# Optimization experiments

Measured on AMD Instinct MI355X. Metric: run time of the kernel, lower is better.

## Reference

```python
import jax, jax.numpy as jnp
import numpy as np

B, L, E = 8, 2048, 4096
TOKEN_DIM, EDGE_DIM, HIDDEN = 768, 256, 128


def setup_inputs() -> dict:
    key = jax.random.key(0)
    k1, k2, k3, k4, k5 = jax.random.split(key, 5)
    token_embedding = jax.random.normal(k1, (B, L, TOKEN_DIM), dtype=jnp.float32)
    edge_embedding = jax.random.normal(k2, (B, E, EDGE_DIM), dtype=jnp.float32)
    # fc: Linear(token_dim+edge_dim -> hidden, bias=False); stored as [in, out]
    W_fc = jax.random.normal(k3, (TOKEN_DIM + EDGE_DIM, HIDDEN), dtype=jnp.float32) * 0.02
    # attn_fc: Linear(2*hidden -> 1); weight flattened to [2*hidden], plus scalar bias
    a_attn = jax.random.normal(k4, (2 * HIDDEN,), dtype=jnp.float32) * 0.02
    b_attn = jax.random.normal(k5, (1,), dtype=jnp.float32) * 0.02
    return {"token_embedding": token_embedding, "edge_embedding": edge_embedding,
            "W_fc": W_fc, "a_attn": a_attn, "b_attn": b_attn}


def reference(token_embedding, edge_embedding, W_fc, a_attn, b_attn):
    # avg edge embedding, broadcast over sequence
    avg_edge = edge_embedding.mean(axis=1, keepdims=True)          # [B, 1, De]
    avg_edge = jnp.broadcast_to(avg_edge, (token_embedding.shape[0],
                                           token_embedding.shape[1],
                                           avg_edge.shape[-1]))     # [B, L, De]
    combined = jnp.concatenate([token_embedding, avg_edge], axis=-1)  # [B, L, Dt+De]
    h = jnp.einsum('bld,dh->blh', combined, W_fc)                   # [B, L, H]

    # Additive attention decomposition: a^T [h_j || h_i] = a1.h_j + a2.h_i
    # (original builds concat([h_repeat_row (=h_j), h_repeat_col (=h_i)]))
    H = h.shape[-1]
    a1, a2 = a_attn[:H], a_attn[H:]
    s_j = jnp.einsum('blh,h->bl', h, a1)                            # score contrib from h_j
    s_i = jnp.einsum('blh,h->bl', h, a2)                            # score contrib from h_i
    scores = s_i[:, :, None] + s_j[:, None, :] + b_attn[0]          # [B, L, L], scores[b,i,j]
    attn = jax.nn.softmax(scores, axis=-1)                          # softmax over j
    h_prime = jnp.einsum('bij,bjh->bih', attn, h)                   # [B, L, H]
    return h_prime
```

## Files before the change

kernel.cpp:

```cpp
#include <hip/hip_runtime.h>

constexpr int Bn  = 8;
constexpr int Ln  = 2048;
constexpr int En  = 4096;
constexpr int TDn = 768;
constexpr int EDn = 256;
constexpr int Hn  = 128;

constexpr int OFF_V1   = 0;
constexpr int OFF_TREC = 1024;
constexpr int TRECF    = 772;
constexpr int OFF_EREC = OFF_TREC + 512 * TRECF;

__global__ __launch_bounds__(256)
void K_0(const float* __restrict__ W, const float* __restrict__ a,
         float* __restrict__ ws)
{
    const int tid = threadIdx.x, wv = tid >> 6, lane = tid & 63;
    int d = blockIdx.x * 4 + wv;
    float acc = W[d * Hn + lane]      * a[lane]
              + W[d * Hn + 64 + lane] * a[64 + lane];
    #pragma unroll
    for (int off = 32; off > 0; off >>= 1)
        acc += __shfl_down(acc, off, 64);
    if (lane == 0) ws[OFF_V1 + d] = acc;
}

__global__ __launch_bounds__(256)
void K_1(const float* __restrict__ token, const float* __restrict__ edge,
         float* __restrict__ ws)
{
    const int tid = threadIdx.x, wv = tid >> 6, lane = tid & 63;
    const int bi = blockIdx.x;
    __shared__ __align__(16) float4 smf[4 * 192];
    __shared__ float sm_den[4];

    if (bi < 512) {
        const int b = bi >> 6, chunk = bi & 63;
        const size_t row0 = (size_t)b * Ln + chunk * 32 + wv * 8;

        const float4* v1_4 = (const float4*)(ws + OFF_V1);
        float4 u0 = v1_4[lane], u1 = v1_4[64 + lane], u2 = v1_4[128 + lane];

        float4 a0 = {0,0,0,0}, a1 = {0,0,0,0}, a2 = {0,0,0,0};
        float esum = 0.f;
        const float4* t4 = (const float4*)token + row0 * (TDn / 4);
        #pragma unroll
        for (int i = 0; i < 8; ++i) {
            float4 v0 = t4[i * 192 + lane];
            float4 v1 = t4[i * 192 + 64 + lane];
            float4 v2 = t4[i * 192 + 128 + lane];
            float d = v0.x*u0.x + v0.y*u0.y + v0.z*u0.z + v0.w*u0.w
                    + v1.x*u1.x + v1.y*u1.y + v1.z*u1.z + v1.w*u1.w
                    + v2.x*u2.x + v2.y*u2.y + v2.z*u2.z + v2.w*u2.w;
            #pragma unroll
            for (int off = 32; off > 0; off >>= 1)
                d += __shfl_xor(d, off, 64);
            float e = expf(d);
            esum += e;
            a0.x += e*v0.x; a0.y += e*v0.y; a0.z += e*v0.z; a0.w += e*v0.w;
            a1.x += e*v1.x; a1.y += e*v1.y; a1.z += e*v1.z; a1.w += e*v1.w;
            a2.x += e*v2.x; a2.y += e*v2.y; a2.z += e*v2.z; a2.w += e*v2.w;
        }
        smf[wv * 192 + lane]       = a0;
        smf[wv * 192 + 64 + lane]  = a1;
        smf[wv * 192 + 128 + lane] = a2;
        if (lane == 0) sm_den[wv] = esum;
        __syncthreads();

        float* rec = ws + OFF_TREC + (size_t)bi * TRECF;
        if (tid < 192) {
            float4 r  = smf[tid];
            float4 r1 = smf[192 + tid], r2 = smf[384 + tid], r3 = smf[576 + tid];
            r.x += r1.x + r2.x + r3.x;  r.y += r1.y + r2.y + r3.y;
            r.z += r1.z + r2.z + r3.z;  r.w += r1.w + r2.w + r3.w;
            ((float4*)(rec + 4))[tid] = r;
        }
        if (tid == 0)
            rec[0] = sm_den[0] + sm_den[1] + sm_den[2] + sm_den[3];
    } else {
        const int eb = bi - 512;
        const int b = eb >> 6, chunk = eb & 63;
        const size_t row0 = (size_t)b * En + chunk * 64 + wv * 16;
        const float4* e4 = (const float4*)edge + row0 * (EDn / 4) + lane;
        float4 acc = {0,0,0,0};
        #pragma unroll
        for (int i = 0; i < 16; ++i) {
            float4 v = e4[(size_t)i * (EDn / 4)];
            acc.x += v.x; acc.y += v.y; acc.z += v.z; acc.w += v.w;
        }
        smf[wv * 64 + lane] = acc;
        __syncthreads();
        if (tid < 64) {
            float4 r0 = smf[tid],       r1 = smf[64 + tid],
                   r2 = smf[128 + tid], r3 = smf[192 + tid];
            float4 s = {r0.x + r1.x + r2.x + r3.x, r0.y + r1.y + r2.y + r3.y,
                        r0.z + r1.z + r2.z + r3.z, r0.w + r1.w + r2.w + r3.w};
            ((float4*)(ws + OFF_EREC))[(size_t)eb * 64 + tid] = s;
        }
    }
}

__global__ __launch_bounds__(256)
void K_2(const float* __restrict__ W, const float* __restrict__ ws,
         float4* __restrict__ out)
{
    __shared__ __align__(16) float s_c[1024];
    __shared__ __align__(16) float4 smp[256];
    __shared__ __align__(16) float4 s_row[32];
    __shared__ float s_den;
    const int tid = threadIdx.x;
    const int b = blockIdx.x >> 5, slice = blockIdx.x & 31;

    float dpart = (tid < 64)
        ? ws[OFF_TREC + (size_t)(b * 64 + tid) * TRECF] : 0.f;

    float4 acc = {0,0,0,0};
    if (tid < 192) {
        const float4* rb = (const float4*)(ws + OFF_TREC)
                         + (size_t)(b * 64) * (TRECF / 4) + 1 + tid;
        #pragma unroll 8
        for (int k = 0; k < 64; ++k) {
            float4 v = rb[(size_t)k * (TRECF / 4)];
            acc.x += v.x; acc.y += v.y; acc.z += v.z; acc.w += v.w;
        }
    } else {
        const float4* rb = (const float4*)(ws + OFF_EREC)
                         + (size_t)(b * 64) * (EDn / 4) + (tid - 192);
        #pragma unroll 8
        for (int k = 0; k < 64; ++k) {
            float4 v = rb[(size_t)k * (EDn / 4)];
            acc.x += v.x; acc.y += v.y; acc.z += v.z; acc.w += v.w;
        }
    }
    if (tid < 64) {
        #pragma unroll
        for (int off = 32; off > 0; off >>= 1)
            dpart += __shfl_xor(dpart, off, 64);
        if (tid == 0) s_den = dpart;
    }
    __syncthreads();

    float scale = (tid < 192) ? (1.0f / s_den) : (1.0f / En);
    float4 c = {acc.x * scale, acc.y * scale, acc.z * scale, acc.w * scale};
    ((float4*)s_c)[tid] = c;
    __syncthreads();

    const int hq = tid & 31, dg = tid >> 5;
    const float4* W4 = (const float4*)W;
    const float* cp = s_c + dg * 128;
    float4 m = {0,0,0,0};
    #pragma unroll 8
    for (int i = 0; i < 128; ++i) {
        float cv = cp[i];
        float4 w = W4[(size_t)(dg * 128 + i) * (Hn / 4) + hq];
        m.x += cv * w.x; m.y += cv * w.y; m.z += cv * w.z; m.w += cv * w.w;
    }
    smp[tid] = m;
    __syncthreads();
    if (tid < 32) {
        float4 r = smp[tid];
        #pragma unroll
        for (int g = 1; g < 8; ++g) {
            float4 v = smp[g * 32 + tid];
            r.x += v.x; r.y += v.y; r.z += v.z; r.w += v.w;
        }
        s_row[tid] = r;
    }
    __syncthreads();

    float4* ob = out + ((size_t)b * Ln + slice * 64) * (Hn / 4);
    #pragma unroll
    for (int k = 0; k < 8; ++k) {
        int f = k * 256 + tid;
        ob[f] = s_row[f & 31];
    }
}

extern "C" void kernel_launch(void* const* d_in, const int* in_sizes, int n_in,
                              void* d_out, int out_size, void* d_ws, size_t ws_size,
                              hipStream_t stream) {
    const float* token = (const float*)d_in[0];
    const float* edge  = (const float*)d_in[1];
    const float* W     = (const float*)d_in[2];
    const float* a     = (const float*)d_in[3];
    float* ws   = (float*)d_ws;
    float4* out = (float4*)d_out;

    K_0<<<192,  256, 0, stream>>>(W, a, ws);
    K_1<<<1024, 256, 0, stream>>>(token, edge, ws);
    K_2<<<256,  256, 0, stream>>>(W, ws, out);
}
```

Before: 128.9 us.

## Fuse token and edge work into uniform blocks with batched loads

K_1 stops splitting blocks into token-only and edge-only branches. Each of the 1024 blocks now handles 16 token rows and 32 edge rows, issues all its token loads up front, and runs four independent dot-product and shuffle reductions together to expose more memory-level parallelism. Because the number of partial records per batch doubles, K_2 reduces 128 records per batch and runs with fewer blocks that each write more output rows. The aim is better load balance and latency hiding in the bandwidth-bound pass, at the cost of a longer reduction in K_2 and more register pressure.

```diff
diff --git a/kernel.cpp b/kernel.cpp
--- a/kernel.cpp
+++ b/kernel.cpp
@@ -10,7 +10,7 @@
 constexpr int OFF_V1   = 0;
 constexpr int OFF_TREC = 1024;
 constexpr int TRECF    = 772;
-constexpr int OFF_EREC = OFF_TREC + 512 * TRECF;
+constexpr int OFF_EREC = OFF_TREC + 1024 * TRECF;
 
 __global__ __launch_bounds__(256)
 void K_0(const float* __restrict__ W, const float* __restrict__ a,
@@ -26,78 +26,108 @@
     if (lane == 0) ws[OFF_V1 + d] = acc;
 }
 
-__global__ __launch_bounds__(256)
+__global__ __launch_bounds__(256, 4)
 void K_1(const float* __restrict__ token, const float* __restrict__ edge,
          float* __restrict__ ws)
 {
     const int tid = threadIdx.x, wv = tid >> 6, lane = tid & 63;
     const int bi = blockIdx.x;
+    const int b = bi >> 7, chunk = bi & 127;
     __shared__ __align__(16) float4 smf[4 * 192];
+    __shared__ __align__(16) float4 sme[4 * 64];
     __shared__ float sm_den[4];
 
-    if (bi < 512) {
-        const int b = bi >> 6, chunk = bi & 63;
-        const size_t row0 = (size_t)b * Ln + chunk * 32 + wv * 8;
-
-        const float4* v1_4 = (const float4*)(ws + OFF_V1);
-        float4 u0 = v1_4[lane], u1 = v1_4[64 + lane], u2 = v1_4[128 + lane];
-
-        float4 a0 = {0,0,0,0}, a1 = {0,0,0,0}, a2 = {0,0,0,0};
-        float esum = 0.f;
-        const float4* t4 = (const float4*)token + row0 * (TDn / 4);
-        #pragma unroll
-        for (int i = 0; i < 8; ++i) {
-            float4 v0 = t4[i * 192 + lane];
-            float4 v1 = t4[i * 192 + 64 + lane];
-            float4 v2 = t4[i * 192 + 128 + lane];
-            float d = v0.x*u0.x + v0.y*u0.y + v0.z*u0.z + v0.w*u0.w
-                    + v1.x*u1.x + v1.y*u1.y + v1.z*u1.z + v1.w*u1.w
-                    + v2.x*u2.x + v2.y*u2.y + v2.z*u2.z + v2.w*u2.w;
-            #pragma unroll
-            for (int off = 32; off > 0; off >>= 1)
-                d += __shfl_xor(d, off, 64);
-            float e = expf(d);
-            esum += e;
-            a0.x += e*v0.x; a0.y += e*v0.y; a0.z += e*v0.z; a0.w += e*v0.w;
-            a1.x += e*v1.x; a1.y += e*v1.y; a1.z += e*v1.z; a1.w += e*v1.w;
-            a2.x += e*v2.x; a2.y += e*v2.y; a2.z += e*v2.z; a2.w += e*v2.w;
-        }
-        smf[wv * 192 + lane]       = a0;
-        smf[wv * 192 + 64 + lane]  = a1;
-        smf[wv * 192 + 128 + lane] = a2;
-        if (lane == 0) sm_den[wv] = esum;
-        __syncthreads();
-
-        float* rec = ws + OFF_TREC + (size_t)bi * TRECF;
-        if (tid < 192) {
-            float4 r  = smf[tid];
-            float4 r1 = smf[192 + tid], r2 = smf[384 + tid], r3 = smf[576 + tid];
-            r.x += r1.x + r2.x + r3.x;  r.y += r1.y + r2.y + r3.y;
-            r.z += r1.z + r2.z + r3.z;  r.w += r1.w + r2.w + r3.w;
-            ((float4*)(rec + 4))[tid] = r;
-        }
-        if (tid == 0)
-            rec[0] = sm_den[0] + sm_den[1] + sm_den[2] + sm_den[3];
-    } else {
-        const int eb = bi - 512;
-        const int b = eb >> 6, chunk = eb & 63;
-        const size_t row0 = (size_t)b * En + chunk * 64 + wv * 16;
-        const float4* e4 = (const float4*)edge + row0 * (EDn / 4) + lane;
-        float4 acc = {0,0,0,0};
-        #pragma unroll
-        for (int i = 0; i < 16; ++i) {
-            float4 v = e4[(size_t)i * (EDn / 4)];
-            acc.x += v.x; acc.y += v.y; acc.z += v.z; acc.w += v.w;
-        }
-        smf[wv * 64 + lane] = acc;
-        __syncthreads();
-        if (tid < 64) {
-            float4 r0 = smf[tid],       r1 = smf[64 + tid],
-                   r2 = smf[128 + tid], r3 = smf[192 + tid];
-            float4 s = {r0.x + r1.x + r2.x + r3.x, r0.y + r1.y + r2.y + r3.y,
-                        r0.z + r1.z + r2.z + r3.z, r0.w + r1.w + r2.w + r3.w};
-            ((float4*)(ws + OFF_EREC))[(size_t)eb * 64 + tid] = s;
-        }
+    const float4* v1_4 = (const float4*)(ws + OFF_V1);
+    float4 u0 = v1_4[lane], u1 = v1_4[64 + lane], u2 = v1_4[128 + lane];
+
+    const size_t trow0 = (size_t)b * Ln + chunk * 16 + wv * 4;
+    const float4* t4 = (const float4*)token + trow0 * (TDn / 4);
+    float4 r0[4], r1[4], r2[4];
+    #pragma unroll
+    for (int i = 0; i < 4; ++i) {
+        r0[i] = t4[i * 192 + lane];
+        r1[i] = t4[i * 192 + 64 + lane];
+        r2[i] = t4[i * 192 + 128 + lane];
+    }
+
+    float d0, d1, d2, d3;
+    {
+        float4 *p;
+        p = &r0[0];
+        d0 = p->x*u0.x + p->y*u0.y + p->z*u0.z + p->w*u0.w;
+        p = &r1[0]; d0 += p->x*u1.x + p->y*u1.y + p->z*u1.z + p->w*u1.w;
+        p = &r2[0]; d0 += p->x*u2.x + p->y*u2.y + p->z*u2.z + p->w*u2.w;
+        p = &r0[1];
+        d1 = p->x*u0.x + p->y*u0.y + p->z*u0.z + p->w*u0.w;
+        p = &r1[1]; d1 += p->x*u1.x + p->y*u1.y + p->z*u1.z + p->w*u1.w;
+        p = &r2[1]; d1 += p->x*u2.x + p->y*u2.y + p->z*u2.z + p->w*u2.w;
+        p = &r0[2];
+        d2 = p->x*u0.x + p->y*u0.y + p->z*u0.z + p->w*u0.w;
+        p = &r1[2]; d2 += p->x*u1.x + p->y*u1.y + p->z*u1.z + p->w*u1.w;
+        p = &r2[2]; d2 += p->x*u2.x + p->y*u2.y + p->z*u2.z + p->w*u2.w;
+        p = &r0[3];
+        d3 = p->x*u0.x + p->y*u0.y + p->z*u0.z + p->w*u0.w;
+        p = &r1[3]; d3 += p->x*u1.x + p->y*u1.y + p->z*u1.z + p->w*u1.w;
+        p = &r2[3]; d3 += p->x*u2.x + p->y*u2.y + p->z*u2.z + p->w*u2.w;
+    }
+    #pragma unroll
+    for (int off = 32; off > 0; off >>= 1) {
+        d0 += __shfl_xor(d0, off, 64);
+        d1 += __shfl_xor(d1, off, 64);
+        d2 += __shfl_xor(d2, off, 64);
+        d3 += __shfl_xor(d3, off, 64);
+    }
+    float e0 = expf(d0), e1 = expf(d1), e2 = expf(d2), e3 = expf(d3);
+    float esum = e0 + e1 + e2 + e3;
+
+    float4 a0, a1, a2;
+    a0.x = e0*r0[0].x + e1*r0[1].x + e2*r0[2].x + e3*r0[3].x;
+    a0.y = e0*r0[0].y + e1*r0[1].y + e2*r0[2].y + e3*r0[3].y;
+    a0.z = e0*r0[0].z + e1*r0[1].z + e2*r0[2].z + e3*r0[3].z;
+    a0.w = e0*r0[0].w + e1*r0[1].w + e2*r0[2].w + e3*r0[3].w;
+    a1.x = e0*r1[0].x + e1*r1[1].x + e2*r1[2].x + e3*r1[3].x;
+    a1.y = e0*r1[0].y + e1*r1[1].y + e2*r1[2].y + e3*r1[3].y;
+    a1.z = e0*r1[0].z + e1*r1[1].z + e2*r1[2].z + e3*r1[3].z;
+    a1.w = e0*r1[0].w + e1*r1[1].w + e2*r1[2].w + e3*r1[3].w;
+    a2.x = e0*r2[0].x + e1*r2[1].x + e2*r2[2].x + e3*r2[3].x;
+    a2.y = e0*r2[0].y + e1*r2[1].y + e2*r2[2].y + e3*r2[3].y;
+    a2.z = e0*r2[0].z + e1*r2[1].z + e2*r2[2].z + e3*r2[3].z;
+    a2.w = e0*r2[0].w + e1*r2[1].w + e2*r2[2].w + e3*r2[3].w;
+
+    const size_t erow0 = (size_t)b * En + chunk * 32 + wv * 8;
+    const float4* e4 = (const float4*)edge + erow0 * (EDn / 4) + lane;
+    float4 eb0 = e4[0],       eb1 = e4[64],      eb2 = e4[128],
+           eb3 = e4[192],     eb4 = e4[256],     eb5 = e4[320],
+           eb6 = e4[384],     eb7 = e4[448];
+    float4 ea;
+    ea.x = ((eb0.x+eb1.x)+(eb2.x+eb3.x)) + ((eb4.x+eb5.x)+(eb6.x+eb7.x));
+    ea.y = ((eb0.y+eb1.y)+(eb2.y+eb3.y)) + ((eb4.y+eb5.y)+(eb6.y+eb7.y));
+    ea.z = ((eb0.z+eb1.z)+(eb2.z+eb3.z)) + ((eb4.z+eb5.z)+(eb6.z+eb7.z));
+    ea.w = ((eb0.w+eb1.w)+(eb2.w+eb3.w)) + ((eb4.w+eb5.w)+(eb6.w+eb7.w));
+
+    smf[wv * 192 + lane]       = a0;
+    smf[wv * 192 + 64 + lane]  = a1;
+    smf[wv * 192 + 128 + lane] = a2;
+    sme[wv * 64 + lane] = ea;
+    if (lane == 0) sm_den[wv] = esum;
+    __syncthreads();
+
+    float* rec = ws + OFF_TREC + (size_t)bi * TRECF;
+    if (tid < 192) {
+        float4 r  = smf[tid];
+        float4 q1 = smf[192 + tid], q2 = smf[384 + tid], q3 = smf[576 + tid];
+        r.x += q1.x + q2.x + q3.x;  r.y += q1.y + q2.y + q3.y;
+        r.z += q1.z + q2.z + q3.z;  r.w += q1.w + q2.w + q3.w;
+        ((float4*)(rec + 4))[tid] = r;
+    }
+    if (tid == 0)
+        rec[0] = sm_den[0] + sm_den[1] + sm_den[2] + sm_den[3];
+    if (tid < 64) {
+        float4 s0 = sme[tid],       s1 = sme[64 + tid],
+               s2 = sme[128 + tid], s3 = sme[192 + tid];
+        float4 s = {s0.x + s1.x + s2.x + s3.x, s0.y + s1.y + s2.y + s3.y,
+                    s0.z + s1.z + s2.z + s3.z, s0.w + s1.w + s2.w + s3.w};
+        ((float4*)(ws + OFF_EREC))[(size_t)bi * 64 + tid] = s;
     }
 }
 
@@ -108,40 +138,41 @@
     __shared__ __align__(16) float s_c[1024];
     __shared__ __align__(16) float4 smp[256];
     __shared__ __align__(16) float4 s_row[32];
-    __shared__ float s_den;
-    const int tid = threadIdx.x;
-    const int b = blockIdx.x >> 5, slice = blockIdx.x & 31;
-
-    float dpart = (tid < 64)
-        ? ws[OFF_TREC + (size_t)(b * 64 + tid) * TRECF] : 0.f;
+    __shared__ float s_den2[2];
+    const int tid = threadIdx.x, wv = tid >> 6, lane = tid & 63;
+    const int b = blockIdx.x >> 4, slice = blockIdx.x & 15;
+
+    float dv = 0.f;
+    if (tid < 128) {
+        dv = ws[OFF_TREC + (size_t)(b * 128 + tid) * TRECF];
+        #pragma unroll
+        for (int off = 32; off > 0; off >>= 1)
+            dv += __shfl_xor(dv, off, 64);
+        if (lane == 0) s_den2[wv] = dv;
+    }
 
     float4 acc = {0,0,0,0};
     if (tid < 192) {
         const float4* rb = (const float4*)(ws + OFF_TREC)
-                         + (size_t)(b * 64) * (TRECF / 4) + 1 + tid;
+                         + (size_t)(b * 128) * (TRECF / 4) + 1 + tid;
         #pragma unroll 8
-        for (int k = 0; k < 64; ++k) {
+        for (int k = 0; k < 128; ++k) {
             float4 v = rb[(size_t)k * (TRECF / 4)];
             acc.x += v.x; acc.y += v.y; acc.z += v.z; acc.w += v.w;
         }
     } else {
         const float4* rb = (const float4*)(ws + OFF_EREC)
-                         + (size_t)(b * 64) * (EDn / 4) + (tid - 192);
+                         + (size_t)(b * 128) * (EDn / 4) + (tid - 192);
         #pragma unroll 8
-        for (int k = 0; k < 64; ++k) {
+        for (int k = 0; k < 128; ++k) {
             float4 v = rb[(size_t)k * (EDn / 4)];
             acc.x += v.x; acc.y += v.y; acc.z += v.z; acc.w += v.w;
         }
     }
-    if (tid < 64) {
-        #pragma unroll
-        for (int off = 32; off > 0; off >>= 1)
-            dpart += __shfl_xor(dpart, off, 64);
-        if (tid == 0) s_den = dpart;
-    }
-    __syncthreads();
-
-    float scale = (tid < 192) ? (1.0f / s_den) : (1.0f / En);
+    __syncthreads();
+
+    float scale = (tid < 192) ? (1.0f / (s_den2[0] + s_den2[1]))
+                              : (1.0f / En);
     float4 c = {acc.x * scale, acc.y * scale, acc.z * scale, acc.w * scale};
     ((float4*)s_c)[tid] = c;
     __syncthreads();
@@ -169,9 +200,9 @@
     }
     __syncthreads();
 
-    float4* ob = out + ((size_t)b * Ln + slice * 64) * (Hn / 4);
-    #pragma unroll
-    for (int k = 0; k < 8; ++k) {
+    float4* ob = out + ((size_t)b * Ln + slice * 128) * (Hn / 4);
+    #pragma unroll
+    for (int k = 0; k < 16; ++k) {
         int f = k * 256 + tid;
         ob[f] = s_row[f & 31];
     }
@@ -189,5 +220,5 @@
 
     K_0<<<192,  256, 0, stream>>>(W, a, ws);
     K_1<<<1024, 256, 0, stream>>>(token, edge, ws);
-    K_2<<<256,  256, 0, stream>>>(W, ws, out);
-}
+    K_2<<<128,  256, 0, stream>>>(W, ws, out);
+}
```

Measured after the change: 133.4 us. 1.03x slower.
